# Kernel tuning notes

Hardware: AMD Instinct MI355X
Metric: run time of the kernel (lower is better)

The kernel has to match this reference:

```python
import jax, jax.numpy as jnp
import numpy as np

BOUND = 1.0
MIN_NEAR = 0.05
NUM_STEPS = 64
UP_STEPS = 64
DENSITY_SCALE = 1.0
N_RAYS = 16384
HIDDEN = 64


def setup_inputs() -> dict:
    key = jax.random.key(0)
    ks = jax.random.split(key, 8)
    # cameras hover near z=2 looking roughly toward -z so rays hit the [-1,1]^3 AABB
    rays_o = jax.random.normal(ks[0], (N_RAYS, 3), jnp.float32) * 0.1 + jnp.array([0.0, 0.0, 2.0])
    rays_d = jax.random.normal(ks[1], (N_RAYS, 3), jnp.float32) * 0.2 + jnp.array([0.0, 0.0, -1.0])
    rays_d = rays_d / jnp.linalg.norm(rays_d, axis=-1, keepdims=True)
    W1 = jax.random.normal(ks[2], (3, HIDDEN), jnp.float32) / jnp.sqrt(3.0)
    b1 = jnp.zeros((HIDDEN,), jnp.float32)
    w_sigma = jax.random.normal(ks[3], (HIDDEN, 1), jnp.float32) / jnp.sqrt(float(HIDDEN))
    b_sigma = jnp.zeros((1,), jnp.float32)
    W_rgb = jax.random.normal(ks[4], (HIDDEN, 3), jnp.float32) / jnp.sqrt(float(HIDDEN))
    b_rgb = jnp.zeros((3,), jnp.float32)
    return {"rays_o": rays_o, "rays_d": rays_d, "W1": W1, "b1": b1,
            "w_sigma": w_sigma, "b_sigma": b_sigma, "W_rgb": W_rgb, "b_rgb": b_rgb}


def near_far_cube(rays_o, rays_d, bound, min_near):
    tmin = (-bound - rays_o) / (rays_d + 1e-15)
    tmax = (bound - rays_o) / (rays_d + 1e-15)
    near = jnp.max(jnp.minimum(tmin, tmax), axis=-1, keepdims=True)
    far = jnp.min(jnp.maximum(tmin, tmax), axis=-1, keepdims=True)
    miss = far < near
    near = jnp.where(miss, 1e9, near)
    far = jnp.where(miss, 1e9, far)
    near = jnp.maximum(near, min_near)
    return near, far


def sample_pdf(bins, weights, n_samples):
    # bins: [N, M+1], weights: [N, M]; deterministic (det=True) inverse-CDF sampling
    weights = weights + 1e-5
    pdf = weights / jnp.sum(weights, -1, keepdims=True)
    cdf = jnp.cumsum(pdf, -1)
    cdf = jnp.concatenate([jnp.zeros_like(cdf[..., :1]), cdf], -1)  # [N, M+1]
    u = jnp.linspace(0.5 / n_samples, 1.0 - 0.5 / n_samples, n_samples, dtype=cdf.dtype)
    u = jnp.broadcast_to(u, cdf.shape[:-1] + (n_samples,))
    inds = jax.vmap(lambda c, uu: jnp.searchsorted(c, uu, side='right'))(cdf, u)
    below = jnp.maximum(inds - 1, 0)
    above = jnp.minimum(inds, cdf.shape[-1] - 1)
    cdf_b = jnp.take_along_axis(cdf, below, -1)
    cdf_a = jnp.take_along_axis(cdf, above, -1)
    bins_b = jnp.take_along_axis(bins, below, -1)
    bins_a = jnp.take_along_axis(bins, above, -1)
    denom = cdf_a - cdf_b
    denom = jnp.where(denom < 1e-5, jnp.ones_like(denom), denom)
    t = (u - cdf_b) / denom
    return bins_b + t * (bins_a - bins_b)


def mlp(pts, W1, b1, w_sigma, b_sigma, W_rgb, b_rgb):
    h = jax.nn.relu(pts @ W1 + b1)                      # [N, T, HIDDEN]
    sigma = jax.nn.softplus(h @ w_sigma + b_sigma)[..., 0]  # [N, T]
    rgb = jax.nn.sigmoid(h @ W_rgb + b_rgb)             # [N, T, 3]
    return sigma, rgb


def alpha_composite_weights(z_vals, sigma, sample_dist):
    deltas = z_vals[..., 1:] - z_vals[..., :-1]
    deltas = jnp.concatenate([deltas, jnp.broadcast_to(sample_dist, deltas[..., :1].shape)], -1)
    alphas = 1.0 - jnp.exp(-deltas * DENSITY_SCALE * sigma)
    trans = jnp.cumprod(jnp.concatenate([jnp.ones_like(alphas[..., :1]), 1.0 - alphas + 1e-15], -1)[..., :-1], -1)
    return alphas * trans


def reference(rays_o, rays_d, W1, b1, w_sigma, b_sigma, W_rgb, b_rgb):
    rays_d = rays_d / jnp.linalg.norm(rays_d, axis=-1, keepdims=True)
    near, far = near_far_cube(rays_o, rays_d, BOUND, MIN_NEAR)  # [N,1]
    sample_dist = (far - near) / NUM_STEPS                      # [N,1]

    # coarse stratified (deterministic) samples
    z = jnp.linspace(0.0, 1.0, NUM_STEPS, dtype=rays_o.dtype)
    z_vals = near + (far - near) * z                            # [N,T]
    xyzs = rays_o[:, None, :] + rays_d[:, None, :] * z_vals[..., None]
    xyzs = jnp.clip(xyzs, -BOUND, BOUND)
    sigma, _ = mlp(xyzs, W1, b1, w_sigma, b_sigma, W_rgb, b_rgb)
    weights = alpha_composite_weights(z_vals, sigma, sample_dist)

    # inverse-CDF importance resampling (no-grad in original)
    z_mid = 0.5 * (z_vals[..., :-1] + z_vals[..., 1:])          # [N,T-1]
    new_z = sample_pdf(z_mid, weights[:, 1:-1], UP_STEPS)       # [N,UP]
    new_z = jax.lax.stop_gradient(new_z)

    z_all = jnp.sort(jnp.concatenate([z_vals, new_z], -1), -1)  # [N,T+UP]
    xyzs_all = rays_o[:, None, :] + rays_d[:, None, :] * z_all[..., None]
    xyzs_all = jnp.clip(xyzs_all, -BOUND, BOUND)
    sigma_all, rgb_all = mlp(xyzs_all, W1, b1, w_sigma, b_sigma, W_rgb, b_rgb)
    weights_all = alpha_composite_weights(z_all, sigma_all, sample_dist)

    weights_sum = jnp.sum(weights_all, -1)                      # [N]
    image = jnp.sum(weights_all[..., None] * rgb_all, axis=-2)  # [N,3]
    image = image + (1.0 - weights_sum)[..., None]              # white background
    return image
```

## Files before the change

kernel.cpp:

```cpp
#include <hip/hip_runtime.h>
#include <math.h>

#define WAVES_PER_BLOCK 4

typedef float v2f __attribute__((ext_vector_type(2)));
typedef float v4f __attribute__((ext_vector_type(4)));
typedef __fp16 fp16v2 __attribute__((ext_vector_type(2)));
typedef _Float16 half8 __attribute__((ext_vector_type(8)));

__device__ __forceinline__ v2f v2_fma(v2f a, v2f b, v2f c) {
    return __builtin_elementwise_fma(a, b, c);
}
__device__ __forceinline__ v2f v2_max0(v2f a) {
    return __builtin_elementwise_max(a, (v2f){0.0f, 0.0f});
}
__device__ __forceinline__ v2f v2_splat(float x) { return (v2f){x, x}; }

__device__ __forceinline__ float fast_rcp(float x) { return __builtin_amdgcn_rcpf(x); }

#define DPP_ROW_SHR(n)  (0x110 | (n))
#define DPP_WF_SL1      0x130
#define DPP_WF_SR1      0x138
#define DPP_ROW_BCAST15 0x142
#define DPP_ROW_BCAST31 0x143

template <int CTRL, int RM = 0xf, int BM = 0xf, bool BC = false>
__device__ __forceinline__ float fdpp(float old_, float src) {
    return __int_as_float(__builtin_amdgcn_update_dpp(
        __float_as_int(old_), __float_as_int(src), CTRL, RM, BM, BC));
}

__device__ __forceinline__ float lane63_bcast(float x) {
    return __int_as_float(__builtin_amdgcn_readlane(__float_as_int(x), 63));
}

__device__ __forceinline__ float scan_add_dpp(float x) {
    x += fdpp<DPP_ROW_SHR(1)>(0.0f, x);
    x += fdpp<DPP_ROW_SHR(2)>(0.0f, x);
    x += fdpp<DPP_ROW_SHR(4)>(0.0f, x);
    x += fdpp<DPP_ROW_SHR(8)>(0.0f, x);
    x += fdpp<DPP_ROW_BCAST15, 0xa>(0.0f, x);
    x += fdpp<DPP_ROW_BCAST31, 0xc>(0.0f, x);
    return x;
}
__device__ __forceinline__ float scan_mul_dpp(float x) {
    x *= fdpp<DPP_ROW_SHR(1)>(1.0f, x);
    x *= fdpp<DPP_ROW_SHR(2)>(1.0f, x);
    x *= fdpp<DPP_ROW_SHR(4)>(1.0f, x);
    x *= fdpp<DPP_ROW_SHR(8)>(1.0f, x);
    x *= fdpp<DPP_ROW_BCAST15, 0xa>(1.0f, x);
    x *= fdpp<DPP_ROW_BCAST31, 0xc>(1.0f, x);
    return x;
}
__device__ __forceinline__ float wave_sum_dpp(float x) {
    return lane63_bcast(scan_add_dpp(x));
}

__device__ __forceinline__ float softplus_f(float x) {
    return fmaxf(x, 0.0f) + __logf(1.0f + __expf(-fabsf(x)));
}
__device__ __forceinline__ float sigmoid_f(float x) {
    return fast_rcp(1.0f + __expf(-x));
}
__device__ __forceinline__ float clamp1(float x) {
    return fminf(fmaxf(x, -1.0f), 1.0f);
}

__device__ __forceinline__ int count_lt64(const float* a, float x) {
    int lo = 0, hi = 64;
    while (lo < hi) { int mid = (lo + hi) >> 1; if (a[mid] < x) lo = mid + 1; else hi = mid; }
    return lo;
}
__device__ __forceinline__ int count_le64(const float* a, float x) {
    int lo = 0, hi = 64;
    while (lo < hi) { int mid = (lo + hi) >> 1; if (a[mid] <= x) lo = mid + 1; else hi = mid; }
    return lo;
}

__global__ __launch_bounds__(WAVES_PER_BLOCK * 64, 8)
void nerf_render_kernel(const float* __restrict__ rays_o,
                        const float* __restrict__ rays_d,
                        const float* __restrict__ W1,
                        const float* __restrict__ b1,
                        const float* __restrict__ w_sigma,
                        const float* __restrict__ b_sigma,
                        const float* __restrict__ W_rgb,
                        const float* __restrict__ b_rgb,
                        float* __restrict__ out)
{
    const int tid  = threadIdx.x;
    const int lane = tid & 63;
    const int wv   = tid >> 6;
    const int ray  = blockIdx.x * WAVES_PER_BLOCK + wv;
    const int r15  = lane & 15;
    const int kgrp = lane >> 4;

    __shared__ float s_cm  [WAVES_PER_BLOCK][128];
    __shared__ float s_zmid[WAVES_PER_BLOCK][64];
    __shared__ float s_cdf [WAVES_PER_BLOCK][64];
    __shared__ float s_zall[WAVES_PER_BLOCK][128];
    __shared__ float s_out [WAVES_PER_BLOCK][4 * 132];

    half8 bfrag[2];
#pragma unroll
    for (int q = 0; q < 2; ++q) {
#pragma unroll
        for (int j = 0; j < 8; ++j) {
            int k = q * 32 + kgrp * 8 + j;
            float wval = 0.0f;
            if (r15 == 0)      wval = w_sigma[k];
            else if (r15 < 4)  wval = W_rgb[3 * k + (r15 - 1)];
            bfrag[q][j] = (_Float16)wval;
        }
    }

    float ox = rays_o[ray * 3 + 0], oy = rays_o[ray * 3 + 1], oz = rays_o[ray * 3 + 2];
    float dx = rays_d[ray * 3 + 0], dy = rays_d[ray * 3 + 1], dz = rays_d[ray * 3 + 2];
    {
        float inv = __builtin_amdgcn_rsqf(dx * dx + dy * dy + dz * dz);
        dx *= inv; dy *= inv; dz *= inv;
    }

    float rx = fast_rcp(dx + 1e-15f);
    float ry = fast_rcp(dy + 1e-15f);
    float rz = fast_rcp(dz + 1e-15f);
    float t0x = (-1.0f - ox) * rx, t1x = (1.0f - ox) * rx;
    float t0y = (-1.0f - oy) * ry, t1y = (1.0f - oy) * ry;
    float t0z = (-1.0f - oz) * rz, t1z = (1.0f - oz) * rz;
    float nearv = fmaxf(fmaxf(fminf(t0x, t1x), fminf(t0y, t1y)), fminf(t0z, t1z));
    float farv  = fminf(fminf(fmaxf(t0x, t1x), fmaxf(t0y, t1y)), fmaxf(t0z, t1z));
    const bool miss = (farv < nearv);
    if (miss) { nearv = 1e9f; farv = 1e9f; }
    nearv = fmaxf(nearv, 0.05f);
    const float sample_dist = (farv - nearv) * (1.0f / 64.0f);

    const float bs0 = b_sigma[0];
    const float br0 = b_rgb[0], br1 = b_rgb[1], br2 = b_rgb[2];

    {
        float w1x = W1[lane], w1y = W1[64 + lane], w1z = W1[128 + lane];
        float eox = ox, eoy = oy, eoz = oz, msc = 1.0f;
        if (miss) {
            eox = clamp1(fmaf(dx, 1e9f, ox));
            eoy = clamp1(fmaf(dy, 1e9f, oy));
            eoz = clamp1(fmaf(dz, 1e9f, oz));
            msc = 0.0f;
        }
        float cj = fmaf(eox, w1x, fmaf(eoy, w1y, fmaf(eoz, w1z, b1[lane])));
        float mj = msc * fmaf(dx, w1x, fmaf(dy, w1y, dz * w1z));
        int g = (lane >> 1) * 4 + (lane & 1);
        s_cm[wv][g]     = cj;
        s_cm[wv][g + 2] = mj;
    }

    float z = nearv + (farv - nearv) * ((float)lane * (1.0f / 63.0f));

    const v2f* ws2 = (const v2f*)w_sigma;
    v2f z2c = v2_splat(z);
    v2f acc0 = (v2f){bs0, 0.0f};
#pragma unroll 8
    for (int t = 0; t < 32; ++t) {
        v4f g = *(const v4f*)&s_cm[wv][4 * t];
        v2f h = v2_max0(v2_fma((v2f){g.z, g.w}, z2c, (v2f){g.x, g.y}));
        acc0 = v2_fma(h, ws2[t], acc0);
    }
    float sigma = softplus_f(acc0.x + acc0.y);

    float z_next = fdpp<DPP_WF_SL1>(0.0f, z);
    float delta  = (lane < 63) ? (z_next - z) : sample_dist;
    float alpha  = 1.0f - __expf(-delta * sigma);
    float v      = 1.0f - alpha + 1e-15f;
    float incl   = scan_mul_dpp(v);
    float trans  = fdpp<DPP_WF_SR1>(1.0f, incl);
    float w = alpha * trans;

    float wgt = (lane >= 1 && lane <= 62) ? (w + 1e-5f) : 0.0f;
    float cumw = scan_add_dpp(wgt);
    float total = lane63_bcast(cumw);
    float cdf_incl = cumw * fast_rcp(total);

    float zmid = 0.5f * (z + z_next);
    s_zmid[wv][lane] = (lane < 63) ? zmid : 0.0f;
    s_cdf [wv][lane] = (lane < 63) ? cdf_incl : 2.0f;

    float u = 0.0078125f + (float)lane * 0.015625f;
    int ind = count_le64(s_cdf[wv], u);
    int below = ind - 1;
    int above = (ind < 62) ? ind : 62;
    float cb = s_cdf[wv][below], ca = s_cdf[wv][above];
    float bb = s_zmid[wv][below], ba = s_zmid[wv][above];
    float denom = ca - cb;
    if (denom < 1e-5f) denom = 1.0f;
    float t = (u - cb) * fast_rcp(denom);
    float nz = fmaf(t, ba - bb, bb);

    s_zmid[wv][lane] = z;
    s_cdf [wv][lane] = nz;
    int pa = lane + count_lt64(s_cdf [wv], z);
    int pb = lane + count_le64(s_zmid[wv], nz);
    s_zall[wv][pa] = z;
    s_zall[wv][pb] = nz;

    float za0 = s_zall[wv][2 * lane + 0];
    float za1 = s_zall[wv][2 * lane + 1];

    {
        float biasv = (r15 == 0) ? bs0 : (r15 == 1) ? br0 : (r15 == 2) ? br1
                     : (r15 == 3) ? br2 : 0.0f;
        v4f accInit = (v4f){biasv, biasv, biasv, biasv};
#pragma unroll 2
        for (int mt = 0; mt < 8; ++mt) {
            const int Mbase = mt * 16;
            float zs = s_zall[wv][Mbase + r15];
            v2f zz = v2_splat(zs);
            v4f acc = accInit;
#pragma unroll
            for (int q = 0; q < 2; ++q) {
                half8 afrag;
#pragma unroll
                for (int g4 = 0; g4 < 4; ++g4) {
                    v4f g = *(const v4f*)&s_cm[wv][4 * (q * 16 + kgrp * 4 + g4)];
                    v2f hp = v2_max0(v2_fma((v2f){g.z, g.w}, zz, (v2f){g.x, g.y}));
                    fp16v2 pk = __builtin_amdgcn_cvt_pkrtz(hp.x, hp.y);
                    afrag[2 * g4]     = (_Float16)pk.x;
                    afrag[2 * g4 + 1] = (_Float16)pk.y;
                }
                acc = __builtin_amdgcn_mfma_f32_16x16x32_f16(afrag, bfrag[q], acc, 0, 0, 0);
            }
            if (r15 < 4) {
                *(v4f*)&s_out[wv][r15 * 132 + Mbase + kgrp * 4] = acc;
            }
        }
    }

    v2f sgp = *(const v2f*)&s_out[wv][0 * 132 + 2 * lane];
    v2f rp  = *(const v2f*)&s_out[wv][1 * 132 + 2 * lane];
    v2f gp  = *(const v2f*)&s_out[wv][2 * 132 + 2 * lane];
    v2f bp  = *(const v2f*)&s_out[wv][3 * 132 + 2 * lane];

    float sg0 = softplus_f(sgp.x), sg1 = softplus_f(sgp.y);
    float r0 = sigmoid_f(rp.x),   r1 = sigmoid_f(rp.y);
    float g0 = sigmoid_f(gp.x),   g1 = sigmoid_f(gp.y);
    float bl0 = sigmoid_f(bp.x),  bl1 = sigmoid_f(bp.y);

    float zn0 = fdpp<DPP_WF_SL1>(0.0f, za0);
    float d0 = za1 - za0;
    float d1 = (lane < 63) ? (zn0 - za1) : sample_dist;
    float a0 = 1.0f - __expf(-d0 * sg0);
    float a1 = 1.0f - __expf(-d1 * sg1);
    float v0 = 1.0f - a0 + 1e-15f;
    float v1 = 1.0f - a1 + 1e-15f;
    float local = v0 * v1;
    float incl2 = scan_mul_dpp(local);
    float eprod = fdpp<DPP_WF_SR1>(1.0f, incl2);
    float w0 = a0 * eprod;
    float w1 = a1 * (eprod * v0);

    float wsum = wave_sum_dpp(w0 + w1);
    float rs   = wave_sum_dpp(fmaf(w0, r0,  w1 * r1));
    float gs   = wave_sum_dpp(fmaf(w0, g0,  w1 * g1));
    float bs   = wave_sum_dpp(fmaf(w0, bl0, w1 * bl1));

    if (lane == 0) {
        float bg = 1.0f - wsum;
        out[ray * 3 + 0] = rs + bg;
        out[ray * 3 + 1] = gs + bg;
        out[ray * 3 + 2] = bs + bg;
    }
}

extern "C" void kernel_launch(void* const* d_in, const int* in_sizes, int n_in,
                              void* d_out, int out_size, void* d_ws, size_t ws_size,
                              hipStream_t stream) {
    const float* rays_o  = (const float*)d_in[0];
    const float* rays_d  = (const float*)d_in[1];
    const float* W1      = (const float*)d_in[2];
    const float* b1      = (const float*)d_in[3];
    const float* w_sigma = (const float*)d_in[4];
    const float* b_sigma = (const float*)d_in[5];
    const float* W_rgb   = (const float*)d_in[6];
    const float* b_rgb   = (const float*)d_in[7];
    float* out = (float*)d_out;

    const int n_rays = in_sizes[0] / 3;
    dim3 grid((n_rays + WAVES_PER_BLOCK - 1) / WAVES_PER_BLOCK);
    dim3 block(WAVES_PER_BLOCK * 64);
    hipLaunchKernelGGL(nerf_render_kernel, grid, block, 0, stream,
                       rays_o, rays_d, W1, b1, w_sigma, b_sigma, W_rgb, b_rgb, out);
}
```

Baseline: 99.23 us.

## Move coarse-pass sigma MLP onto MFMA and hoist hidden-layer coefficients into registers

The first-pass sigma evaluation used to be a 32-step scalar FMA loop per lane. It now runs through the same 16x16x32 f16 MFMA path as the fine pass, and results go to a new shared array. The per-lane c/m coefficients are loaded from LDS once into registers (cr/mr) and reused by both passes, which removes repeated LDS reads inside the loops. The launch-bounds occupancy hint drops from 8 to 4 so the extra registers fit. z inputs are clamped to 6e4 to avoid fp16 overflow for missed rays, and the coarse sigma now carries fp16 rounding error.

After: 98.73 us. Within noise of the previous version (-0.5%).

```diff
diff --git a/kernel.cpp b/kernel.cpp
--- a/kernel.cpp
+++ b/kernel.cpp
@@ -77,7 +77,17 @@
     return lo;
 }
 
-__global__ __launch_bounds__(WAVES_PER_BLOCK * 64, 8)
+__device__ __forceinline__ half8 build_afrag(const v2f* cr, const v2f* mr, v2f zz, int q) {
+    union { half8 h; fp16v2 p[4]; } af;
+#pragma unroll
+    for (int g4 = 0; g4 < 4; ++g4) {
+        v2f hp = v2_max0(v2_fma(mr[q * 4 + g4], zz, cr[q * 4 + g4]));
+        af.p[g4] = __builtin_amdgcn_cvt_pkrtz(hp.x, hp.y);
+    }
+    return af.h;
+}
+
+__global__ __launch_bounds__(WAVES_PER_BLOCK * 64, 4)
 void nerf_render_kernel(const float* __restrict__ rays_o,
                         const float* __restrict__ rays_d,
                         const float* __restrict__ W1,
@@ -96,6 +106,7 @@
     const int kgrp = lane >> 4;
 
     __shared__ float s_cm  [WAVES_PER_BLOCK][128];
+    __shared__ float s_sig [WAVES_PER_BLOCK][64];
     __shared__ float s_zmid[WAVES_PER_BLOCK][64];
     __shared__ float s_cdf [WAVES_PER_BLOCK][64];
     __shared__ float s_zall[WAVES_PER_BLOCK][128];
@@ -153,18 +164,36 @@
         s_cm[wv][g + 2] = mj;
     }
 
+    v2f cr[8], mr[8];
+#pragma unroll
+    for (int q = 0; q < 2; ++q) {
+#pragma unroll
+        for (int g4 = 0; g4 < 4; ++g4) {
+            v4f g = *(const v4f*)&s_cm[wv][4 * (q * 16 + kgrp * 4 + g4)];
+            cr[q * 4 + g4] = (v2f){g.x, g.y};
+            mr[q * 4 + g4] = (v2f){g.z, g.w};
+        }
+    }
+
+    const float biasv = (r15 == 0) ? bs0 : (r15 == 1) ? br0 : (r15 == 2) ? br1
+                       : (r15 == 3) ? br2 : 0.0f;
+    const v4f accInit = (v4f){biasv, biasv, biasv, biasv};
+
+    const float stepz = (farv - nearv) * (1.0f / 63.0f);
+#pragma unroll
+    for (int mt = 0; mt < 4; ++mt) {
+        float zs = fminf(fmaf(stepz, (float)(mt * 16 + r15), nearv), 6.0e4f);
+        v2f zz = v2_splat(zs);
+        v4f acc = accInit;
+        acc = __builtin_amdgcn_mfma_f32_16x16x32_f16(build_afrag(cr, mr, zz, 0), bfrag[0], acc, 0, 0, 0);
+        acc = __builtin_amdgcn_mfma_f32_16x16x32_f16(build_afrag(cr, mr, zz, 1), bfrag[1], acc, 0, 0, 0);
+        if (r15 == 0) {
+            *(v4f*)&s_sig[wv][mt * 16 + kgrp * 4] = acc;
+        }
+    }
+    float sigma = softplus_f(s_sig[wv][lane]);
+
     float z = nearv + (farv - nearv) * ((float)lane * (1.0f / 63.0f));
-
-    const v2f* ws2 = (const v2f*)w_sigma;
-    v2f z2c = v2_splat(z);
-    v2f acc0 = (v2f){bs0, 0.0f};
-#pragma unroll 8
-    for (int t = 0; t < 32; ++t) {
-        v4f g = *(const v4f*)&s_cm[wv][4 * t];
-        v2f h = v2_max0(v2_fma((v2f){g.z, g.w}, z2c, (v2f){g.x, g.y}));
-        acc0 = v2_fma(h, ws2[t], acc0);
-    }
-    float sigma = softplus_f(acc0.x + acc0.y);
 
     float z_next = fdpp<DPP_WF_SL1>(0.0f, z);
     float delta  = (lane < 63) ? (z_next - z) : sample_dist;
@@ -204,32 +233,16 @@
     float za0 = s_zall[wv][2 * lane + 0];
     float za1 = s_zall[wv][2 * lane + 1];
 
-    {
-        float biasv = (r15 == 0) ? bs0 : (r15 == 1) ? br0 : (r15 == 2) ? br1
-                     : (r15 == 3) ? br2 : 0.0f;
-        v4f accInit = (v4f){biasv, biasv, biasv, biasv};
 #pragma unroll 2
-        for (int mt = 0; mt < 8; ++mt) {
-            const int Mbase = mt * 16;
-            float zs = s_zall[wv][Mbase + r15];
-            v2f zz = v2_splat(zs);
-            v4f acc = accInit;
-#pragma unroll
-            for (int q = 0; q < 2; ++q) {
-                half8 afrag;
-#pragma unroll
-                for (int g4 = 0; g4 < 4; ++g4) {
-                    v4f g = *(const v4f*)&s_cm[wv][4 * (q * 16 + kgrp * 4 + g4)];
-                    v2f hp = v2_max0(v2_fma((v2f){g.z, g.w}, zz, (v2f){g.x, g.y}));
-                    fp16v2 pk = __builtin_amdgcn_cvt_pkrtz(hp.x, hp.y);
-                    afrag[2 * g4]     = (_Float16)pk.x;
-                    afrag[2 * g4 + 1] = (_Float16)pk.y;
-                }
-                acc = __builtin_amdgcn_mfma_f32_16x16x32_f16(afrag, bfrag[q], acc, 0, 0, 0);
-            }
-            if (r15 < 4) {
-                *(v4f*)&s_out[wv][r15 * 132 + Mbase + kgrp * 4] = acc;
-            }
+    for (int mt = 0; mt < 8; ++mt) {
+        const int Mbase = mt * 16;
+        float zs = fminf(s_zall[wv][Mbase + r15], 6.0e4f);
+        v2f zz = v2_splat(zs);
+        v4f acc = accInit;
+        acc = __builtin_amdgcn_mfma_f32_16x16x32_f16(build_afrag(cr, mr, zz, 0), bfrag[0], acc, 0, 0, 0);
+        acc = __builtin_amdgcn_mfma_f32_16x16x32_f16(build_afrag(cr, mr, zz, 1), bfrag[1], acc, 0, 0, 0);
+        if (r15 < 4) {
+            *(v4f*)&s_out[wv][r15 * 132 + Mbase + kgrp * 4] = acc;
         }
     }
 
```
